# Performance work log

Hardware: AMD Instinct MI355X
Metric: run time of the kernel (lower is better)

The kernel has to match this reference:

```python
import jax, jax.numpy as jnp
import numpy as np

EMBED_DIM = 1024
NUM_HEADS = 16


def setup_inputs() -> dict:
    key = jax.random.key(0)
    k_x, k_w, k_b, k_ow, k_ob = jax.random.split(key, 5)
    B, S, E = 4, 2048, EMBED_DIM
    scale = 1.0 / np.sqrt(E)
    x = jax.random.normal(k_x, (B, S, E), dtype=jnp.float32)
    # nn.MultiheadAttention packed in-projection [3E, E] and out projection [E, E]
    in_proj_w = jax.random.uniform(k_w, (3 * E, E), dtype=jnp.float32, minval=-scale, maxval=scale)
    in_proj_b = jnp.zeros((3 * E,), dtype=jnp.float32)
    out_proj_w = jax.random.uniform(k_ow, (E, E), dtype=jnp.float32, minval=-scale, maxval=scale)
    out_proj_b = jnp.zeros((E,), dtype=jnp.float32)
    return {"x": x, "in_proj_w": in_proj_w, "in_proj_b": in_proj_b,
            "out_proj_w": out_proj_w, "out_proj_b": out_proj_b}


def reference(x, in_proj_w, in_proj_b, out_proj_w, out_proj_b):
    B, S, E = x.shape
    H = NUM_HEADS
    hd = E // H
    # packed QKV projection: [B,S,3E]
    qkv = x @ in_proj_w.T + in_proj_b
    q, k, v = jnp.split(qkv, 3, axis=-1)
    # [B,S,E] -> [B,H,S,hd]
    def to_heads(t):
        return t.reshape(B, S, H, hd).transpose(0, 2, 1, 3)
    q, k, v = to_heads(q), to_heads(k), to_heads(v)
    scale = 1.0 / jnp.sqrt(jnp.asarray(hd, dtype=x.dtype))
    scores = jnp.einsum('bhqd,bhkd->bhqk', q * scale, k)  # [B,H,S,S]
    # causal mask: position i attends to <= i (matches the -inf additive mask)
    causal = jnp.tril(jnp.ones((S, S), dtype=bool))
    scores = jnp.where(causal[None, None, :, :], scores, jnp.finfo(x.dtype).min)
    attn = jax.nn.softmax(scores, axis=-1)
    out = jnp.einsum('bhqk,bhkd->bhqd', attn, v)  # [B,H,S,hd]
    out = out.transpose(0, 2, 1, 3).reshape(B, S, E)
    return out @ out_proj_w.T + out_proj_b
```

## Files before the change

kernel.cpp:

```cpp
#include <hip/hip_runtime.h>
#include <stdint.h>

typedef _Float16 f16;
typedef _Float16 f16x2 __attribute__((ext_vector_type(2)));
typedef _Float16 f16x8 __attribute__((ext_vector_type(8)));
typedef float f32x4 __attribute__((ext_vector_type(4)));
typedef float f32x16 __attribute__((ext_vector_type(16)));
typedef uint32_t u32x4 __attribute__((ext_vector_type(4)));

#define B_   4
#define S_   2048
#define E_   1024
#define H_   16
#define HD_  64
#define BH_  (B_ * H_)

template <int N> struct IC { static constexpr int v = N; };

__device__ __forceinline__ void async_lds16(const void* g, void* l) {
    __builtin_amdgcn_global_load_lds(
        (__attribute__((address_space(1))) void*)(uintptr_t)g,
        (__attribute__((address_space(3))) void*)(uint32_t)(uintptr_t)l,
        16, 0, 0);
}

__global__ __launch_bounds__(256)
void cvt_f32_to_f16(const float* __restrict__ in, f16* __restrict__ out, int n8) {
    int i = blockIdx.x * 256 + threadIdx.x;
    if (i >= n8) return;
    const float4* p = (const float4*)in;
    float4 a = p[2 * i], b = p[2 * i + 1];
    f16x8 o;
    o[0] = (f16)a.x; o[1] = (f16)a.y; o[2] = (f16)a.z; o[3] = (f16)a.w;
    o[4] = (f16)b.x; o[5] = (f16)b.y; o[6] = (f16)b.z; o[7] = (f16)b.w;
    *(f16x8*)(out + 8 * (long)i) = o;
}

__global__ __launch_bounds__(512)
void gemm_qkv(const f16* __restrict__ A, const f16* __restrict__ Bm,
              const float* __restrict__ bias,
              f16* __restrict__ qo, f16* __restrict__ ko, f16* __restrict__ vto)
{
    constexpr int K = 1024, N = 3072, NT = 16;
    __shared__ __align__(16) f16 L[3][(128 + 256) * 64];
    const int tid = threadIdx.x, wave = tid >> 6, lane = tid & 63;
    const int lo = lane & 15, hi = lane >> 4;
    const int bid0 = blockIdx.x;
    const int bid = (bid0 & 7) * 96 + (bid0 >> 3);
    const int tm = bid / 12, tn = bid % 12;
    const long bm0 = (long)tm * 128, bn0 = (long)tn * 256;
    const int wr = (wave >> 2) * 64, wc = (wave & 3) * 64;

#define STAGE6(BUF, T)  do {                                                      \
    const long kk = (long)(T) * 64;                                               \
    _Pragma("unroll")                                                             \
    for (int j = 0; j < 2; ++j) {                                                 \
        const int c = j * 512 + tid;                                              \
        const int row = c >> 3, ch = c & 7;                                       \
        async_lds16(A + (bm0 + row) * K + kk + ((ch ^ (row & 7)) * 8),            \
                    &L[BUF][(j * 512 + wave * 64) * 8]);                          \
    }                                                                             \
    _Pragma("unroll")                                                             \
    for (int j = 0; j < 4; ++j) {                                                 \
        const int c = j * 512 + tid;                                              \
        const int row = c >> 3, ch = c & 7;                                       \
        async_lds16(Bm + (bn0 + row) * K + kk + ((ch ^ (row & 7)) * 8),           \
                    &L[BUF][8192 + (j * 512 + wave * 64) * 8]);                   \
    } } while (0)

    f32x4 acc[4][4] = {};

    auto tile = [&](auto bufc, int t) {
        constexpr int BUF = decltype(bufc)::v;
        constexpr int SBUF = (BUF + 2) % 3;
        if (t + 2 < NT) STAGE6(SBUF, t + 2);
        f16x8 af[2][4], bf[2][4];
#pragma unroll
        for (int kh = 0; kh < 2; ++kh) {
#pragma unroll
            for (int mi = 0; mi < 4; ++mi) {
                const int r = wr + mi * 16 + lo;
                af[kh][mi] = *(const f16x8*)&L[BUF][(r * 8 + ((kh * 4 + hi) ^ (r & 7))) * 8];
            }
#pragma unroll
            for (int ni = 0; ni < 4; ++ni) {
                const int r = wc + ni * 16 + lo;
                bf[kh][ni] = *(const f16x8*)&L[BUF][8192 + (r * 8 + ((kh * 4 + hi) ^ (r & 7))) * 8];
            }
        }
        __builtin_amdgcn_s_setprio(1);
#pragma unroll
        for (int kh = 0; kh < 2; ++kh)
#pragma unroll
            for (int mi = 0; mi < 4; ++mi)
#pragma unroll
                for (int ni = 0; ni < 4; ++ni)
                    acc[mi][ni] = __builtin_amdgcn_mfma_f32_16x16x32_f16(
                        af[kh][mi], bf[kh][ni], acc[mi][ni], 0, 0, 0);
        __builtin_amdgcn_s_setprio(0);
        if (t + 2 < NT) asm volatile("s_waitcnt vmcnt(6)" ::: "memory");
        else            asm volatile("s_waitcnt vmcnt(0)" ::: "memory");
        __builtin_amdgcn_sched_barrier(0);
        __builtin_amdgcn_s_barrier();
    };

    STAGE6(0, 0);
    STAGE6(1, 1);
    asm volatile("s_waitcnt vmcnt(6)" ::: "memory");
    __builtin_amdgcn_sched_barrier(0);
    __builtin_amdgcn_s_barrier();
    for (int t = 0; t < 15; t += 3) {
        tile(IC<0>{}, t);
        tile(IC<1>{}, t + 1);
        tile(IC<2>{}, t + 2);
    }
    tile(IC<0>{}, 15);
#undef STAGE6

    const int which = (int)(bn0 >> 10);
    if (which < 2) {
#pragma unroll
        for (int mi = 0; mi < 4; ++mi)
#pragma unroll
            for (int ni = 0; ni < 4; ++ni)
#pragma unroll
                for (int j = 0; j < 4; ++j) {
                    const long r  = bm0 + wr + mi * 16 + 4 * hi + j;
                    const int  cn = (int)bn0 + wc + ni * 16 + lo;
                    const int  e = cn & 1023, h = e >> 6, d = e & 63;
                    const int  b = (int)(r >> 11), s = (int)(r & 2047);
                    const long bh = (long)b * H_ + h;
                    const f16 hv = (f16)(acc[mi][ni][j] + bias[cn]);
                    if (which == 0) qo[(bh * S_ + s) * HD_ + d] = hv;
                    else            ko[(bh * S_ + s) * HD_ + d] = hv;
                }
    } else {
        f16* T = ((f16*)L) + wave * 4096;
#pragma unroll
        for (int ni = 0; ni < 4; ++ni) {
            const int dl = ni * 16 + lo;
            const int dx = dl & 7;
#pragma unroll
            for (int mi = 0; mi < 4; ++mi)
#pragma unroll
                for (int j = 0; j < 4; ++j) {
                    const int sl = mi * 16 + 4 * hi + j;
                    const int cn = (int)bn0 + wc + ni * 16 + lo;
                    T[dl * 64 + ((((sl >> 3) ^ dx) << 3) | (sl & 7))] =
                        (f16)(acc[mi][ni][j] + bias[cn]);
                }
        }
        const int b = (int)(bm0 >> 11);
        const int sbase = (int)(bm0 & 2047) + wr;
        const int h = ((int)(bn0 & 1023) + wc) >> 6;
        const long vbase = (long)(b * H_ + h) * HD_;
#pragma unroll
        for (int it = 0; it < 8; ++it) {
            const int d = it * 8 + (lane >> 3);
            const int schunk = lane & 7;
            u32x4 val = *(const u32x4*)&T[d * 64 + ((schunk ^ (d & 7)) << 3)];
            *(u32x4*)&vto[(vbase + d) * S_ + sbase + schunk * 8] = val;
        }
    }
}

template <int MODE>
__global__ __launch_bounds__(256)
void gemm_bt(const f16* __restrict__ A, const f16* __restrict__ Bm,
             const float* __restrict__ bias, float* __restrict__ Cf,
             f16* __restrict__ qo, f16* __restrict__ ko, f16* __restrict__ vto,
             int M, int N, int K)
{
    __shared__ __align__(16) f16 As[2][128 * 32];
    __shared__ __align__(16) f16 Bs[2][128 * 32];
    const int tid = threadIdx.x;
    const int wave = tid >> 6, lane = tid & 63;
    const int lo = lane & 15, hi = lane >> 4;
    const int ntn = N >> 7;
    const int tm = blockIdx.x / ntn, tn = blockIdx.x % ntn;
    const long bm0 = (long)tm << 7, bn0 = (long)tn << 7;
    const int wr = (wave >> 1) << 6, wc = (wave & 1) << 6;

    int srow[2], sxc[2];
#pragma unroll
    for (int p = 0; p < 2; ++p) {
        const int c = p * 256 + tid;
        srow[p] = c >> 2;
        sxc[p]  = (((c & 3) ^ ((c >> 3) & 3))) * 8;
    }

#define GSTAGE(BUF, K0)  do {                                                     \
    _Pragma("unroll")                                                             \
    for (int p = 0; p < 2; ++p) {                                                 \
        const int base = (p * 256 + wave * 64) * 8;                               \
        async_lds16(A  + (bm0 + srow[p]) * K + (K0) + sxc[p], &As[BUF][base]);    \
        async_lds16(Bm + (bn0 + srow[p]) * K + (K0) + sxc[p], &Bs[BUF][base]);    \
    } } while (0)

    f32x4 acc[4][4] = {};

    auto compute = [&](auto bufc) {
        constexpr int BUF = decltype(bufc)::v;
        f16x8 af[4], bf[4];
#pragma unroll
        for (int mi = 0; mi < 4; ++mi) {
            const int row = wr + mi * 16 + lo;
            af[mi] = *(const f16x8*)&As[BUF][row * 32 + ((hi ^ ((row >> 1) & 3)) * 8)];
        }
#pragma unroll
        for (int ni = 0; ni < 4; ++ni) {
            const int row = wc + ni * 16 + lo;
            bf[ni] = *(const f16x8*)&Bs[BUF][row * 32 + ((hi ^ ((row >> 1) & 3)) * 8)];
        }
        __builtin_amdgcn_s_setprio(1);
#pragma unroll
        for (int mi = 0; mi < 4; ++mi)
#pragma unroll
            for (int ni = 0; ni < 4; ++ni)
                acc[mi][ni] = __builtin_amdgcn_mfma_f32_16x16x32_f16(
                    af[mi], bf[ni], acc[mi][ni], 0, 0, 0);
        __builtin_amdgcn_s_setprio(0);
    };

    GSTAGE(0, 0);
    __syncthreads();
    for (int k0 = 0; k0 < K; k0 += 64) {
        GSTAGE(1, k0 + 32);
        compute(IC<0>{});
        __syncthreads();
        if (k0 + 64 < K) GSTAGE(0, k0 + 64);
        compute(IC<1>{});
        __syncthreads();
    }
#undef GSTAGE

    if (MODE == 1) {
#pragma unroll
        for (int mi = 0; mi < 4; ++mi)
#pragma unroll
            for (int ni = 0; ni < 4; ++ni)
#pragma unroll
                for (int j = 0; j < 4; ++j) {
                    const long r  = bm0 + wr + mi * 16 + 4 * hi + j;
                    const int  cn = (int)bn0 + wc + ni * 16 + lo;
                    Cf[r * N + cn] = acc[mi][ni][j] + bias[cn];
                }
        return;
    }
    (void)qo; (void)ko; (void)vto;
}

__global__ __launch_bounds__(256)
void attn_fwd(const f16* __restrict__ qb, const f16* __restrict__ kb,
              const f16* __restrict__ vtb, f16* __restrict__ ob)
{
    __shared__ __align__(16) f16 Ks[2][64 * 64];
    __shared__ __align__(16) f16 Vs[2][64 * 64];
    const int tid = threadIdx.x, wave = tid >> 6, lane = tid & 63;
    const int q32 = lane & 31, h2 = lane >> 5;
    const int bh = blockIdx.y;
    const int qtA = blockIdx.x;
    const int qtB = 15 - qtA;
    const int qwA = qtA * 128 + wave * 32;
    const int qwB = qtB * 128 + wave * 32;
    const long krow0 = (long)bh * S_;
    const long vrow0 = (long)bh * HD_;

#define STAGE(BUF, KV)  do {                                                      \
    _Pragma("unroll")                                                             \
    for (int p = 0; p < 2; ++p) {                                                 \
        const int n = p * 256 + tid;                                              \
        const int base = (p * 256 + wave * 64) * 8;                               \
        async_lds16(kb  + (krow0 + (KV) + (n & 63)) * HD_ + (n >> 6) * 8, &Ks[BUF][base]); \
        async_lds16(vtb + (vrow0 + (n & 63)) * S_ + (KV) + (n >> 6) * 8, &Vs[BUF][base]);  \
    } } while (0)

    f16x8 qfA[4], qfB[4];
    const f16 sch = (f16)0.1803368801f;
#pragma unroll
    for (int kkq = 0; kkq < 4; ++kkq) {
        qfA[kkq] = *(const f16x8*)&qb[(krow0 + qwA + q32) * HD_ + kkq * 16 + h2 * 8];
        qfB[kkq] = *(const f16x8*)&qb[(krow0 + qwB + q32) * HD_ + kkq * 16 + h2 * 8];
#pragma unroll
        for (int e = 0; e < 8; ++e) { qfA[kkq][e] *= sch; qfB[kkq][e] *= sch; }
    }

    f32x16 oaccA[2] = {}, oaccB[2] = {};
    float lA = 0.f, lB = 0.f;
    const f16x2 ones2 = { (f16)1.0f, (f16)1.0f };

    auto computeS = [&](auto bufc, auto spc, int t) {
        constexpr int BUF = decltype(bufc)::v;
        constexpr int SP  = decltype(spc)::v;
        const int qw = SP ? qwB : qwA;
        const f16x8* qf = SP ? qfB : qfA;
        f32x16* oacc = SP ? oaccB : oaccA;
        float& l_part = SP ? lB : lA;
        const int kv0 = t * 64;
        if (kv0 > qw + 31) return;
        const int qg = qw + q32;

        f32x16 sc[2] = {};
        __builtin_amdgcn_s_setprio(1);
#pragma unroll
        for (int kkq = 0; kkq < 4; ++kkq)
#pragma unroll
            for (int ni = 0; ni < 2; ++ni) {
                f16x8 kf = *(const f16x8*)&Ks[BUF][(((kkq * 2 + h2) * 64) + ni * 32 + q32) * 8];
                sc[ni] = __builtin_amdgcn_mfma_f32_32x32x16_f16(kf, qf[kkq], sc[ni], 0, 0, 0);
            }
        __builtin_amdgcn_s_setprio(0);

        const bool maskp = (kv0 + 63) > qw;
#pragma unroll
        for (int ni = 0; ni < 2; ++ni)
#pragma unroll
            for (int r = 0; r < 16; ++r) {
                float p = __builtin_amdgcn_exp2f(sc[ni][r]);
                const int kvg = kv0 + ni * 32 + (r & 3) + 8 * (r >> 2) + 4 * h2;
                if (maskp && kvg > qg) p = 0.0f;
                sc[ni][r] = p;
            }

        __builtin_amdgcn_s_setprio(1);
#pragma unroll
        for (int ni = 0; ni < 2; ++ni) {
            uint32_t u[8];
#pragma unroll
            for (int m = 0; m < 8; ++m) {
                auto hp = __builtin_amdgcn_cvt_pkrtz(sc[ni][2 * m], sc[ni][2 * m + 1]);
                u[m] = __builtin_bit_cast(uint32_t, hp);
                l_part = __builtin_amdgcn_fdot2(__builtin_bit_cast(f16x2, u[m]), ones2, l_part, false);
            }
#pragma unroll
            for (int kkv = 0; kkv < 2; ++kkv) {
                auto sA = __builtin_amdgcn_permlane32_swap(u[4 * kkv + 0], u[4 * kkv + 2], false, false);
                auto sB = __builtin_amdgcn_permlane32_swap(u[4 * kkv + 1], u[4 * kkv + 3], false, false);
                u32x4 uv = { (uint32_t)sA[0], (uint32_t)sB[0], (uint32_t)sA[1], (uint32_t)sB[1] };
                f16x8 pf = __builtin_bit_cast(f16x8, uv);
                const int kg = ni * 2 + kkv;
#pragma unroll
                for (int dh = 0; dh < 2; ++dh) {
                    f16x8 vf = *(const f16x8*)&Vs[BUF][(((kg * 2 + h2) * 64) + dh * 32 + q32) * 8];
                    oacc[dh] = __builtin_amdgcn_mfma_f32_32x32x16_f16(pf, vf, oacc[dh], 0, 0, 0);
                }
            }
        }
        __builtin_amdgcn_s_setprio(0);
    };

    const int ntB = 2 * (qtB + 1);
    STAGE(0, 0);
    __syncthreads();
    for (int t = 0; t < ntB; t += 2) {
        STAGE(1, (t + 1) * 64);
        computeS(IC<0>{}, IC<0>{}, t);
        computeS(IC<0>{}, IC<1>{}, t);
        __syncthreads();
        if (t + 2 < ntB) STAGE(0, (t + 2) * 64);
        computeS(IC<1>{}, IC<0>{}, t + 1);
        computeS(IC<1>{}, IC<1>{}, t + 1);
        __syncthreads();
    }
#undef STAGE

    const int b = bh >> 4, h = bh & 15;
    const float invA = 1.0f / (lA + __shfl_xor(lA, 32));
    const float invB = 1.0f / (lB + __shfl_xor(lB, 32));
#pragma unroll
    for (int r = 0; r < 16; ++r) {
        const int crow = (r & 3) + 8 * (r >> 2) + 4 * h2;
        const float irA = __shfl(invA, crow);
        const float irB = __shfl(invB, crow);
#pragma unroll
        for (int dh = 0; dh < 2; ++dh) {
            ob[((long)b * S_ + qwA + crow) * E_ + h * HD_ + dh * 32 + q32] = (f16)(oaccA[dh][r] * irA);
            ob[((long)b * S_ + qwB + crow) * E_ + h * HD_ + dh * 32 + q32] = (f16)(oaccB[dh][r] * irB);
        }
    }
}

extern "C" void kernel_launch(void* const* d_in, const int* in_sizes, int n_in,
                              void* d_out, int out_size, void* d_ws, size_t ws_size,
                              hipStream_t stream)
{
    (void)in_sizes; (void)n_in; (void)out_size; (void)ws_size;
    const float* x  = (const float*)d_in[0];
    const float* w1 = (const float*)d_in[1];
    const float* b1 = (const float*)d_in[2];
    const float* w2 = (const float*)d_in[3];
    const float* b2 = (const float*)d_in[4];
    float* out = (float*)d_out;

    char* ws = (char*)d_ws;
    f16* xb  = (f16*)ws;  ws += (size_t)8192 * 1024 * 2;
    f16* w1b = (f16*)ws;  ws += (size_t)3072 * 1024 * 2;
    f16* w2b = (f16*)ws;  ws += (size_t)1024 * 1024 * 2;
    f16* qb  = (f16*)ws;  ws += (size_t)BH_ * S_ * HD_ * 2;
    f16* kb  = (f16*)ws;  ws += (size_t)BH_ * S_ * HD_ * 2;
    f16* vtb = (f16*)ws;  ws += (size_t)BH_ * S_ * HD_ * 2;
    f16* ao  = (f16*)ws;  ws += (size_t)8192 * 1024 * 2;

    cvt_f32_to_f16<<<dim3(8192 * 1024 / 8 / 256), dim3(256), 0, stream>>>(x,  xb,  8192 * 1024 / 8);
    cvt_f32_to_f16<<<dim3(3072 * 1024 / 8 / 256), dim3(256), 0, stream>>>(w1, w1b, 3072 * 1024 / 8);
    cvt_f32_to_f16<<<dim3(1024 * 1024 / 8 / 256), dim3(256), 0, stream>>>(w2, w2b, 1024 * 1024 / 8);

    gemm_qkv<<<dim3(768), dim3(512), 0, stream>>>(xb, w1b, b1, qb, kb, vtb);

    attn_fwd<<<dim3(8, 64), dim3(256), 0, stream>>>(qb, kb, vtb, ao);

    gemm_bt<1><<<dim3(64 * 8), dim3(256), 0, stream>>>(
        ao, w2b, b2, out, nullptr, nullptr, nullptr, 8192, 1024, 1024);
}
```

Measured before the change: 159.2 us.

## Merge conversion kernels, reuse pipelined GEMM for out-proj, reorder attention grid

The three f32-to-f16 conversion launches become one kernel that picks its source and destination by index range, which removes two launches. The output projection now uses the triple-buffered 128x256 pipelined GEMM kernel instead of the simpler double-buffered 128x128 one. The attention grid is transposed so consecutive blocks cover different (batch, head) pairs for the same query tile. The out-proj launch drops to 256 blocks, which may leave some CUs idle on a large GPU.

```diff
diff --git a/kernel.cpp b/kernel.cpp
--- a/kernel.cpp
+++ b/kernel.cpp
@@ -25,29 +25,40 @@
 }
 
 __global__ __launch_bounds__(256)
-void cvt_f32_to_f16(const float* __restrict__ in, f16* __restrict__ out, int n8) {
-    int i = blockIdx.x * 256 + threadIdx.x;
-    if (i >= n8) return;
-    const float4* p = (const float4*)in;
-    float4 a = p[2 * i], b = p[2 * i + 1];
+void cvt3(const float* __restrict__ x, const float* __restrict__ w1,
+          const float* __restrict__ w2, f16* __restrict__ xb,
+          f16* __restrict__ w1b, f16* __restrict__ w2b)
+{
+    const long i = (long)blockIdx.x * 256 + threadIdx.x;
+    const float* src; f16* dst; long j;
+    if (i < 1048576)      { src = x;  dst = xb;  j = i; }
+    else if (i < 1441792) { src = w1; dst = w1b; j = i - 1048576; }
+    else                  { src = w2; dst = w2b; j = i - 1441792; }
+    const float4* p = (const float4*)src;
+    float4 a = p[2 * j], b = p[2 * j + 1];
     f16x8 o;
     o[0] = (f16)a.x; o[1] = (f16)a.y; o[2] = (f16)a.z; o[3] = (f16)a.w;
     o[4] = (f16)b.x; o[5] = (f16)b.y; o[6] = (f16)b.z; o[7] = (f16)b.w;
-    *(f16x8*)(out + 8 * (long)i) = o;
-}
-
+    *(f16x8*)(dst + 8 * j) = o;
+}
+
+template <int MODE>
 __global__ __launch_bounds__(512)
-void gemm_qkv(const f16* __restrict__ A, const f16* __restrict__ Bm,
-              const float* __restrict__ bias,
-              f16* __restrict__ qo, f16* __restrict__ ko, f16* __restrict__ vto)
+void gemm_pipe(const f16* __restrict__ A, const f16* __restrict__ Bm,
+               const float* __restrict__ bias,
+               f16* __restrict__ qo, f16* __restrict__ ko, f16* __restrict__ vto,
+               float* __restrict__ Cf)
 {
-    constexpr int K = 1024, N = 3072, NT = 16;
+    constexpr int K = 1024, NT = 16;
+    constexpr int N = (MODE == 0) ? 3072 : 1024;
+    constexpr int NTN = N / 256;
+    constexpr int NBLK = 64 * NTN;
     __shared__ __align__(16) f16 L[3][(128 + 256) * 64];
     const int tid = threadIdx.x, wave = tid >> 6, lane = tid & 63;
     const int lo = lane & 15, hi = lane >> 4;
     const int bid0 = blockIdx.x;
-    const int bid = (bid0 & 7) * 96 + (bid0 >> 3);
-    const int tm = bid / 12, tn = bid % 12;
+    const int bid = (bid0 & 7) * (NBLK / 8) + (bid0 >> 3);
+    const int tm = bid / NTN, tn = bid % NTN;
     const long bm0 = (long)tm * 128, bn0 = (long)tn * 256;
     const int wr = (wave >> 2) * 64, wc = (wave & 3) * 64;
 
@@ -117,6 +128,20 @@
     tile(IC<0>{}, 15);
 #undef STAGE6
 
+    if (MODE == 1) {
+#pragma unroll
+        for (int mi = 0; mi < 4; ++mi)
+#pragma unroll
+            for (int ni = 0; ni < 4; ++ni)
+#pragma unroll
+                for (int j = 0; j < 4; ++j) {
+                    const long r  = bm0 + wr + mi * 16 + 4 * hi + j;
+                    const int  cn = (int)bn0 + wc + ni * 16 + lo;
+                    Cf[r * N + cn] = acc[mi][ni][j] + bias[cn];
+                }
+        return;
+    }
+
     const int which = (int)(bn0 >> 10);
     if (which < 2) {
 #pragma unroll
@@ -164,92 +189,6 @@
     }
 }
 
-template <int MODE>
-__global__ __launch_bounds__(256)
-void gemm_bt(const f16* __restrict__ A, const f16* __restrict__ Bm,
-             const float* __restrict__ bias, float* __restrict__ Cf,
-             f16* __restrict__ qo, f16* __restrict__ ko, f16* __restrict__ vto,
-             int M, int N, int K)
-{
-    __shared__ __align__(16) f16 As[2][128 * 32];
-    __shared__ __align__(16) f16 Bs[2][128 * 32];
-    const int tid = threadIdx.x;
-    const int wave = tid >> 6, lane = tid & 63;
-    const int lo = lane & 15, hi = lane >> 4;
-    const int ntn = N >> 7;
-    const int tm = blockIdx.x / ntn, tn = blockIdx.x % ntn;
-    const long bm0 = (long)tm << 7, bn0 = (long)tn << 7;
-    const int wr = (wave >> 1) << 6, wc = (wave & 1) << 6;
-
-    int srow[2], sxc[2];
-#pragma unroll
-    for (int p = 0; p < 2; ++p) {
-        const int c = p * 256 + tid;
-        srow[p] = c >> 2;
-        sxc[p]  = (((c & 3) ^ ((c >> 3) & 3))) * 8;
-    }
-
-#define GSTAGE(BUF, K0)  do {                                                     \
-    _Pragma("unroll")                                                             \
-    for (int p = 0; p < 2; ++p) {                                                 \
-        const int base = (p * 256 + wave * 64) * 8;                               \
-        async_lds16(A  + (bm0 + srow[p]) * K + (K0) + sxc[p], &As[BUF][base]);    \
-        async_lds16(Bm + (bn0 + srow[p]) * K + (K0) + sxc[p], &Bs[BUF][base]);    \
-    } } while (0)
-
-    f32x4 acc[4][4] = {};
-
-    auto compute = [&](auto bufc) {
-        constexpr int BUF = decltype(bufc)::v;
-        f16x8 af[4], bf[4];
-#pragma unroll
-        for (int mi = 0; mi < 4; ++mi) {
-            const int row = wr + mi * 16 + lo;
-            af[mi] = *(const f16x8*)&As[BUF][row * 32 + ((hi ^ ((row >> 1) & 3)) * 8)];
-        }
-#pragma unroll
-        for (int ni = 0; ni < 4; ++ni) {
-            const int row = wc + ni * 16 + lo;
-            bf[ni] = *(const f16x8*)&Bs[BUF][row * 32 + ((hi ^ ((row >> 1) & 3)) * 8)];
-        }
-        __builtin_amdgcn_s_setprio(1);
-#pragma unroll
-        for (int mi = 0; mi < 4; ++mi)
-#pragma unroll
-            for (int ni = 0; ni < 4; ++ni)
-                acc[mi][ni] = __builtin_amdgcn_mfma_f32_16x16x32_f16(
-                    af[mi], bf[ni], acc[mi][ni], 0, 0, 0);
-        __builtin_amdgcn_s_setprio(0);
-    };
-
-    GSTAGE(0, 0);
-    __syncthreads();
-    for (int k0 = 0; k0 < K; k0 += 64) {
-        GSTAGE(1, k0 + 32);
-        compute(IC<0>{});
-        __syncthreads();
-        if (k0 + 64 < K) GSTAGE(0, k0 + 64);
-        compute(IC<1>{});
-        __syncthreads();
-    }
-#undef GSTAGE
-
-    if (MODE == 1) {
-#pragma unroll
-        for (int mi = 0; mi < 4; ++mi)
-#pragma unroll
-            for (int ni = 0; ni < 4; ++ni)
-#pragma unroll
-                for (int j = 0; j < 4; ++j) {
-                    const long r  = bm0 + wr + mi * 16 + 4 * hi + j;
-                    const int  cn = (int)bn0 + wc + ni * 16 + lo;
-                    Cf[r * N + cn] = acc[mi][ni][j] + bias[cn];
-                }
-        return;
-    }
-    (void)qo; (void)ko; (void)vto;
-}
-
 __global__ __launch_bounds__(256)
 void attn_fwd(const f16* __restrict__ qb, const f16* __restrict__ kb,
               const f16* __restrict__ vtb, f16* __restrict__ ob)
@@ -258,8 +197,8 @@
     __shared__ __align__(16) f16 Vs[2][64 * 64];
     const int tid = threadIdx.x, wave = tid >> 6, lane = tid & 63;
     const int q32 = lane & 31, h2 = lane >> 5;
-    const int bh = blockIdx.y;
-    const int qtA = blockIdx.x;
+    const int bh = blockIdx.x;
+    const int qtA = blockIdx.y;
     const int qtB = 15 - qtA;
     const int qwA = qtA * 128 + wave * 32;
     const int qwB = qtB * 128 + wave * 32;
@@ -401,14 +340,11 @@
     f16* vtb = (f16*)ws;  ws += (size_t)BH_ * S_ * HD_ * 2;
     f16* ao  = (f16*)ws;  ws += (size_t)8192 * 1024 * 2;
 
-    cvt_f32_to_f16<<<dim3(8192 * 1024 / 8 / 256), dim3(256), 0, stream>>>(x,  xb,  8192 * 1024 / 8);
-    cvt_f32_to_f16<<<dim3(3072 * 1024 / 8 / 256), dim3(256), 0, stream>>>(w1, w1b, 3072 * 1024 / 8);
-    cvt_f32_to_f16<<<dim3(1024 * 1024 / 8 / 256), dim3(256), 0, stream>>>(w2, w2b, 1024 * 1024 / 8);
-
-    gemm_qkv<<<dim3(768), dim3(512), 0, stream>>>(xb, w1b, b1, qb, kb, vtb);
-
-    attn_fwd<<<dim3(8, 64), dim3(256), 0, stream>>>(qb, kb, vtb, ao);
-
-    gemm_bt<1><<<dim3(64 * 8), dim3(256), 0, stream>>>(
-        ao, w2b, b2, out, nullptr, nullptr, nullptr, 8192, 1024, 1024);
-}
+    cvt3<<<dim3(6144), dim3(256), 0, stream>>>(x, w1, w2, xb, w1b, w2b);
+
+    gemm_pipe<0><<<dim3(768), dim3(512), 0, stream>>>(xb, w1b, b1, qb, kb, vtb, nullptr);
+
+    attn_fwd<<<dim3(64, 8), dim3(256), 0, stream>>>(qb, kb, vtb, ao);
+
+    gemm_pipe<1><<<dim3(256), dim3(512), 0, stream>>>(ao, w2b, b2, nullptr, nullptr, nullptr, out);
+}
```

Result: faster. 148.8 us (median of 5 runs) (-6.5%).
